# Kernel optimization log

Hardware: AMD Instinct MI355X
Metric: run time of the kernel (lower is better)

The kernel has to match this reference:

```python
import jax, jax.numpy as jnp
import numpy as np

HID = 128
N_NODES = 50000
N_EDGES = 640000
N_GRAPHS = 64
N_LAYERS = 3
LN_EPS = 1e-5


def _ln(h, g, b):
    mu = jnp.mean(h, axis=-1, keepdims=True)
    v = jnp.mean(jnp.square(h - mu), axis=-1, keepdims=True)
    return (h - mu) * jax.lax.rsqrt(v + LN_EPS) * g + b


def _mlp2(h, W1, b1, g, be, W2, b2):
    # Linear -> ReLU -> LayerNorm -> (Dropout=identity in eval) -> Linear
    h = _ln(jax.nn.relu(h @ W1.T + b1), g, be)
    return h @ W2.T + b2


def _forward(x, edge_index, batch, axis_W1, axis_b1, axis_g, axis_be, axis_W2, axis_b2, org_W1, org_b1, org_g, org_be, org_W2, org_b2, nin_W, nin_b, conv_W1, conv_b1, conv_g, conv_be, conv_W2, conv_b2, eps, ln_g, ln_b, gate_W1, gate_b1, gate_g, gate_be, gate_W2, gate_b2, head_W1, head_b1, head_g, head_be, head_W2, head_b2):
    axis = x[:, 9:12]
    origin = x[:, 12:15]
    others = jnp.concatenate([x[:, :9], x[:, 15:19]], axis=1)  # [N, 13]
    axis_z = _mlp2(axis, axis_W1, axis_b1, axis_g, axis_be, axis_W2, axis_b2)
    org_z = _mlp2(origin, org_W1, org_b1, org_g, org_be, org_W2, org_b2)
    h = jnp.concatenate([others, axis_z, org_z], axis=1) @ nin_W.T + nin_b  # [N, HID]
    src, dst = edge_index[0], edge_index[1]
    n = x.shape[0]
    for l in range(N_LAYERS):
        res = h
        # GIN: sum-aggregate source features into targets (gather + scatter-add)
        agg = jax.ops.segment_sum(h[src], dst, num_segments=n)
        m = (1.0 + eps[l]) * h + agg
        m = _mlp2(m, conv_W1[l], conv_b1[l], conv_g[l], conv_be[l], conv_W2[l], conv_b2[l])
        h = _ln(jax.nn.relu(m), ln_g[l], ln_b[l]) + res
    # AttentionalAggregation: segment softmax over per-graph node gates
    gate = _mlp2(h, gate_W1, gate_b1, gate_g, gate_be, gate_W2, gate_b2)  # [N, 1]
    gmax = jax.ops.segment_max(gate, batch, num_segments=N_GRAPHS)
    e = jnp.exp(gate - gmax[batch])
    denom = jax.ops.segment_sum(e, batch, num_segments=N_GRAPHS)
    attn = e / denom[batch]
    g = jax.ops.segment_sum(attn * h, batch, num_segments=N_GRAPHS)  # [B, HID]
    logit = _mlp2(g, head_W1, head_b1, head_g, head_be, head_W2, head_b2)[:, 0]
    return logit


def setup_inputs() -> dict:
    key = jax.random.key(0)
    ks = iter(jax.random.split(key, 64))
    nk = lambda: next(ks)
    lin = lambda o, i: jax.random.normal(nk(), (o, i), jnp.float32) / np.float32(np.sqrt(i))
    lin3 = lambda L, o, i: jnp.stack([lin(o, i) for _ in range(L)])
    z = lambda *s: jnp.zeros(s, jnp.float32)
    o = lambda *s: jnp.ones(s, jnp.float32)
    inp = {}
    inp['x'] = jax.random.normal(nk(), (N_NODES, 19), jnp.float32)
    inp['edge_index'] = jax.random.randint(nk(), (2, N_EDGES), 0, N_NODES)
    inp['batch'] = jnp.sort(jax.random.randint(nk(), (N_NODES,), 0, N_GRAPHS))
    for p in ('axis', 'org'):
        inp[p + '_W1'] = lin(16, 3); inp[p + '_b1'] = z(16)
        inp[p + '_g'] = o(16); inp[p + '_be'] = z(16)
        inp[p + '_W2'] = lin(16, 16); inp[p + '_b2'] = z(16)
    inp['nin_W'] = lin(HID, 45); inp['nin_b'] = z(HID)
    inp['conv_W1'] = lin3(N_LAYERS, HID, HID); inp['conv_b1'] = z(N_LAYERS, HID)
    inp['conv_g'] = o(N_LAYERS, HID); inp['conv_be'] = z(N_LAYERS, HID)
    inp['conv_W2'] = lin3(N_LAYERS, HID, HID); inp['conv_b2'] = z(N_LAYERS, HID)
    inp['eps'] = z(N_LAYERS)
    inp['ln_g'] = o(N_LAYERS, HID); inp['ln_b'] = z(N_LAYERS, HID)
    for p in ('gate', 'head'):
        inp[p + '_W1'] = lin(HID // 2, HID); inp[p + '_b1'] = z(HID // 2)
        inp[p + '_g'] = o(HID // 2); inp[p + '_be'] = z(HID // 2)
        inp[p + '_W2'] = lin(1, HID // 2); inp[p + '_b2'] = z(1)
    return inp


def reference(x, edge_index, batch, axis_W1, axis_b1, axis_g, axis_be, axis_W2, axis_b2, org_W1, org_b1, org_g, org_be, org_W2, org_b2, nin_W, nin_b, conv_W1, conv_b1, conv_g, conv_be, conv_W2, conv_b2, eps, ln_g, ln_b, gate_W1, gate_b1, gate_g, gate_be, gate_W2, gate_b2, head_W1, head_b1, head_g, head_be, head_W2, head_b2):
    return _forward(x, edge_index, batch, axis_W1, axis_b1, axis_g, axis_be, axis_W2, axis_b2, org_W1, org_b1, org_g, org_be, org_W2, org_b2, nin_W, nin_b, conv_W1, conv_b1, conv_g, conv_be, conv_W2, conv_b2, eps, ln_g, ln_b, gate_W1, gate_b1, gate_g, gate_be, gate_W2, gate_b2, head_W1, head_b1, head_g, head_be, head_W2, head_b2)
```

## Files before the change

### kernel.cpp

```cpp
#include <hip/hip_runtime.h>

#define N_NODESC 50000
#define N_EDGESC 640000
#define N_GRAPHSC 64
#define HIDC 128
#define LN_EPSF 1e-5f
#define POOL_SPLIT 16
#define SCAN_NB 49
#define EGRID ((N_EDGESC + 255) / 256)
#define NGRID_GB ((N_NODESC + 255) / 256)
#define PREP_ELEMS (8192 + 49152 + 49152)
#define WPREP_NB ((PREP_ELEMS + 255) / 256)

typedef short bf16x8 __attribute__((ext_vector_type(8)));
typedef float f32x4 __attribute__((ext_vector_type(4)));

static __device__ __forceinline__ unsigned ord_enc(float f) {
  unsigned u = __float_as_uint(f);
  return (u & 0x80000000u) ? ~u : (u | 0x80000000u);
}
static __device__ __forceinline__ float ord_dec(unsigned u) {
  return __uint_as_float((u & 0x80000000u) ? (u ^ 0x80000000u) : ~u);
}
static __device__ __forceinline__ unsigned short f2bf(float x) {
  unsigned u = __float_as_uint(x);
  u += 0x7fffu + ((u >> 16) & 1u);
  return (unsigned short)(u >> 16);
}
static __device__ __forceinline__ float bf2f(unsigned short b) {
  return __uint_as_float(((unsigned)b) << 16);
}

static __device__ __forceinline__ void mlp16(float in0, float in1, float in2,
    const float* __restrict__ W1, const float* __restrict__ b1,
    const float* __restrict__ g, const float* __restrict__ be,
    const float* __restrict__ W2, const float* __restrict__ b2,
    float* __restrict__ out) {
  float h[16];
  float s1 = 0.f, s2 = 0.f;
#pragma unroll
  for (int j = 0; j < 16; ++j) {
    float v = b1[j] + W1[j*3+0]*in0 + W1[j*3+1]*in1 + W1[j*3+2]*in2;
    v = fmaxf(v, 0.f);
    h[j] = v; s1 += v; s2 += v*v;
  }
  float mu = s1 * (1.f/16.f);
  float var = fmaxf(s2 * (1.f/16.f) - mu*mu, 0.f);
  float rs = rsqrtf(var + LN_EPSF);
  float z[16];
#pragma unroll
  for (int j = 0; j < 16; ++j) z[j] = (h[j]-mu)*rs*g[j] + be[j];
#pragma unroll
  for (int j = 0; j < 16; ++j) {
    float v = b2[j];
#pragma unroll
    for (int k = 0; k < 16; ++k) v += W2[j*16+k]*z[k];
    out[j] = v;
  }
}

__global__ __launch_bounds__(256) void hist_gbound_kernel(const int* __restrict__ ei,
    int* __restrict__ deg, const int* __restrict__ batch, int* __restrict__ gstart,
    const float* __restrict__ ninW, unsigned short* __restrict__ ninWb,
    const float* __restrict__ cW1, unsigned short* __restrict__ cW1b,
    const float* __restrict__ cW2, unsigned short* __restrict__ cW2b) {
  const int b = blockIdx.x;
  if (b < EGRID) {
    int e = b * 256 + threadIdx.x;
    if (e < N_EDGESC) atomicAdd(&deg[ei[N_EDGESC + e]], 1);
  } else if (b < EGRID + NGRID_GB) {
    int i = (b - EGRID) * 256 + threadIdx.x;
    if (i >= N_NODESC) return;
    int bb = batch[i];
    int prev = (i == 0) ? -1 : batch[i-1];
    for (int g = prev + 1; g <= bb; ++g) gstart[g] = i;
    if (i == N_NODESC - 1) {
      for (int g = bb + 1; g <= N_GRAPHSC; ++g) gstart[g] = N_NODESC;
    }
  } else {
    int i = (b - EGRID - NGRID_GB) * 256 + threadIdx.x;
    if (i < 8192) {
      int f = i >> 6, k = i & 63;
      ninWb[i] = (k < 45) ? f2bf(ninW[f*45 + k]) : (unsigned short)0;
    } else if (i < 8192 + 49152) {
      int j = i - 8192;
      cW1b[j] = f2bf(cW1[j]);
    } else if (i < PREP_ELEMS) {
      int j = i - 8192 - 49152;
      cW2b[j] = f2bf(cW2[j]);
    }
  }
}

__global__ __launch_bounds__(1024) void scan1_kernel(const int* __restrict__ deg,
                                                     int* __restrict__ incl,
                                                     int* __restrict__ bsum) {
  const int b = blockIdx.x, t = threadIdx.x;
  const int i = b * 1024 + t;
  const int lane = t & 63, w = t >> 6;
  int v = (i < N_NODESC) ? deg[i] : 0;
#pragma unroll
  for (int off = 1; off < 64; off <<= 1) {
    int n = __shfl_up(v, off);
    if (lane >= off) v += n;
  }
  __shared__ int wsum[16];
  if (lane == 63) wsum[w] = v;
  __syncthreads();
  if (t == 0) {
    int run = 0;
#pragma unroll
    for (int k = 0; k < 16; ++k) { int x = wsum[k]; wsum[k] = run; run += x; }
  }
  __syncthreads();
  v += wsum[w];
  if (i < N_NODESC) incl[i] = v;
  if (t == 1023) bsum[b] = v;
}

__global__ __launch_bounds__(1024) void scan23_kernel(const int* __restrict__ deg,
                                                      const int* __restrict__ bsum,
                                                      int* __restrict__ rowptr,
                                                      int* __restrict__ cursor) {
  __shared__ int ex[SCAN_NB + 1];
  const int b = blockIdx.x, t = threadIdx.x;
  if (t < 64) {
    int v = (t < SCAN_NB) ? bsum[t] : 0;
    const int orig = v;
#pragma unroll
    for (int off = 1; off < 64; off <<= 1) {
      int n = __shfl_up(v, off);
      if (t >= off) v += n;
    }
    if (t < SCAN_NB) ex[t] = v - orig;
    if (t == SCAN_NB - 1) ex[SCAN_NB] = v;
  }
  __syncthreads();
  const int i = b * 1024 + t;
  if (i < N_NODESC) {
    int excl = rowptr[i] - deg[i] + ex[b];
    rowptr[i] = excl;
    cursor[i] = excl;
  }
  if (b == 0 && t == 0) rowptr[N_NODESC] = ex[SCAN_NB];
}

__global__ __launch_bounds__(256) void scatter_kernel(const int* __restrict__ ei,
                                                      int* __restrict__ cursor,
                                                      int* __restrict__ esrc) {
  int e = blockIdx.x * 256 + threadIdx.x;
  if (e < N_EDGESC) {
    int d = ei[N_EDGESC + e];
    int slot = atomicAdd(&cursor[d], 1);
    esrc[slot] = ei[e];
  }
}

__global__ __launch_bounds__(256, 4) void enc_mfma_kernel(
    const float* __restrict__ x,
    const float* __restrict__ aW1, const float* __restrict__ ab1,
    const float* __restrict__ ag,  const float* __restrict__ abe,
    const float* __restrict__ aW2, const float* __restrict__ ab2,
    const float* __restrict__ oW1, const float* __restrict__ ob1,
    const float* __restrict__ og,  const float* __restrict__ obe,
    const float* __restrict__ oW2, const float* __restrict__ ob2,
    const unsigned short* __restrict__ ninWb, const float* __restrict__ ninb,
    unsigned short* __restrict__ Hb) {
  __shared__ unsigned short Ab[64*136];
  const int t = threadIdx.x;
  const int nb = blockIdx.x * 64;

  if (t < 192) {
    const int n = t & 63;
    const int gn = nb + n;
    const int grp = t >> 6;
    if (gn < N_NODESC) {
      const float* xr = x + gn * 19;
      if (grp == 0) {
        float z[16];
        mlp16(xr[9], xr[10], xr[11], aW1, ab1, ag, abe, aW2, ab2, z);
#pragma unroll
        for (int k = 0; k < 16; ++k) Ab[n*136 + 13 + k] = f2bf(z[k]);
      } else if (grp == 1) {
        float z[16];
        mlp16(xr[12], xr[13], xr[14], oW1, ob1, og, obe, oW2, ob2, z);
#pragma unroll
        for (int k = 0; k < 16; ++k) Ab[n*136 + 29 + k] = f2bf(z[k]);
      } else {
#pragma unroll
        for (int k = 0; k < 9; ++k) Ab[n*136 + k] = f2bf(xr[k]);
#pragma unroll
        for (int k = 0; k < 4; ++k) Ab[n*136 + 9 + k] = f2bf(xr[15 + k]);
#pragma unroll
        for (int k = 45; k < 64; ++k) Ab[n*136 + k] = 0;
      }
    } else {
      if (grp == 0) {
#pragma unroll
        for (int k = 0; k < 16; ++k) Ab[n*136 + 13 + k] = 0;
      } else if (grp == 1) {
#pragma unroll
        for (int k = 0; k < 16; ++k) Ab[n*136 + 29 + k] = 0;
      } else {
#pragma unroll
        for (int k = 0; k < 13; ++k) Ab[n*136 + k] = 0;
#pragma unroll
        for (int k = 45; k < 64; ++k) Ab[n*136 + k] = 0;
      }
    }
  }
  __syncthreads();

  const int lane = t & 63, wv = t >> 6;
  const int quad = lane >> 4, l16 = lane & 15;
  const int arow = (wv*16 + l16)*136 + quad*8;
  f32x4 acc[8];
#pragma unroll
  for (int ft = 0; ft < 8; ++ft) acc[ft] = (f32x4){0.f,0.f,0.f,0.f};
#pragma unroll
  for (int ks = 0; ks < 2; ++ks) {
    bf16x8 a = *(const bf16x8*)(const void*)&Ab[arow + ks*32];
#pragma unroll
    for (int ft = 0; ft < 8; ++ft) {
      bf16x8 bfr = *(const bf16x8*)&ninWb[(ft*16 + l16)*64 + quad*8 + ks*32];
      acc[ft] = __builtin_amdgcn_mfma_f32_16x16x32_bf16(a, bfr, acc[ft], 0, 0, 0);
    }
  }
  float bb[8];
#pragma unroll
  for (int ft = 0; ft < 8; ++ft) bb[ft] = ninb[ft*16 + l16];
  __syncthreads();
#pragma unroll
  for (int r = 0; r < 4; ++r) {
    int nloc = wv*16 + quad*4 + r;
#pragma unroll
    for (int ft = 0; ft < 8; ++ft)
      Ab[nloc*136 + ft*16 + l16] = f2bf(acc[ft][r] + bb[ft]);
  }
  __syncthreads();
#pragma unroll
  for (int i = 0; i < 4; ++i) {
    int chunk = t + i*256;
    int n = chunk >> 4, c8 = chunk & 15;
    int gn = nb + n;
    if (gn < N_NODESC)
      *(bf16x8*)&Hb[gn*HIDC + c8*8] = *(const bf16x8*)&Ab[n*136 + c8*8];
  }
}

__global__ __launch_bounds__(128) void agg_kernel(const unsigned short* __restrict__ Hb,
    const int* __restrict__ rowptr, const int* __restrict__ esrc,
    const float* __restrict__ epsp, unsigned short* __restrict__ Mb) {
  const int t = threadIdx.x;
  const int c8 = t & 15;
  const int v  = t >> 4;
  const int node = blockIdx.x * 8 + v;
  if (node >= N_NODESC) return;
  const float e1 = 1.0f + epsp[0];
  bf16x8 h = *(const bf16x8*)&Hb[node*HIDC + c8*8];
  float acc[8];
#pragma unroll
  for (int k = 0; k < 8; ++k) acc[k] = 0.f;
  int s = rowptr[node];
  const int e = rowptr[node+1];
  for (; s + 4 <= e; s += 4) {
    int i0 = esrc[s], i1 = esrc[s+1], i2 = esrc[s+2], i3 = esrc[s+3];
    bf16x8 x0 = *(const bf16x8*)&Hb[i0*HIDC + c8*8];
    bf16x8 x1 = *(const bf16x8*)&Hb[i1*HIDC + c8*8];
    bf16x8 x2 = *(const bf16x8*)&Hb[i2*HIDC + c8*8];
    bf16x8 x3 = *(const bf16x8*)&Hb[i3*HIDC + c8*8];
#pragma unroll
    for (int k = 0; k < 8; ++k)
      acc[k] += (bf2f((unsigned short)x0[k]) + bf2f((unsigned short)x1[k]))
              + (bf2f((unsigned short)x2[k]) + bf2f((unsigned short)x3[k]));
  }
  for (; s < e; ++s) {
    bf16x8 x0 = *(const bf16x8*)&Hb[esrc[s]*HIDC + c8*8];
#pragma unroll
    for (int k = 0; k < 8; ++k) acc[k] += bf2f((unsigned short)x0[k]);
  }
  bf16x8 m8;
#pragma unroll
  for (int k = 0; k < 8; ++k)
    m8[k] = (short)f2bf(e1*bf2f((unsigned short)h[k]) + acc[k]);
  *(bf16x8*)&Mb[node*HIDC + c8*8] = m8;
}

__global__ __launch_bounds__(256, 3) void gemmpair_kernel(
    const unsigned short* __restrict__ Mb,
    const unsigned short* __restrict__ Hin,
    const unsigned short* __restrict__ W1b, const float* __restrict__ b1,
    const float* __restrict__ g1, const float* __restrict__ be1,
    const unsigned short* __restrict__ W2b, const float* __restrict__ b2,
    const float* __restrict__ lng, const float* __restrict__ lnb,
    unsigned short* __restrict__ Hout) {
  __shared__ unsigned short Ab[64*136];
  __shared__ unsigned short Wl[128*136];
  const int t = threadIdx.x;
  const int nb = blockIdx.x * 64;

#pragma unroll
  for (int i = 0; i < 4; ++i) {
    int chunk = t + i*256;
    int n = chunk >> 4, c8 = chunk & 15;
    int gn = nb + n;
    bf16x8 v = {0,0,0,0,0,0,0,0};
    if (gn < N_NODESC) v = *(const bf16x8*)&Mb[gn*HIDC + c8*8];
    *(bf16x8*)&Ab[n*136 + c8*8] = v;
  }
#pragma unroll
  for (int i = 0; i < 8; ++i) {
    int q = t + i*256;
    int f = q >> 4, c8 = q & 15;
    *(bf16x8*)&Wl[f*136 + c8*8] = *(const bf16x8*)&W1b[f*HIDC + c8*8];
  }
  __syncthreads();

  const int lane = t & 63, wv = t >> 6;
  const int quad = lane >> 4, l16 = lane & 15;
  const int arow = (wv*16 + l16)*136 + quad*8;

  f32x4 acc[8];
#pragma unroll
  for (int ft = 0; ft < 8; ++ft) acc[ft] = (f32x4){0.f,0.f,0.f,0.f};
#pragma unroll
  for (int ks = 0; ks < 4; ++ks) {
    bf16x8 a = *(const bf16x8*)(const void*)&Ab[arow + ks*32];
#pragma unroll
    for (int ft = 0; ft < 8; ++ft) {
      bf16x8 b = *(const bf16x8*)(const void*)&Wl[(ft*16 + l16)*136 + quad*8 + ks*32];
      acc[ft] = __builtin_amdgcn_mfma_f32_16x16x32_bf16(a, b, acc[ft], 0, 0, 0);
    }
  }

  {
    float bb[8], gg[8], bee[8];
#pragma unroll
    for (int ft = 0; ft < 8; ++ft) {
      int f = ft*16 + l16;
      bb[ft] = b1[f]; gg[ft] = g1[f]; bee[ft] = be1[f];
    }
    float s1[4] = {0,0,0,0}, s2[4] = {0,0,0,0};
#pragma unroll
    for (int ft = 0; ft < 8; ++ft)
#pragma unroll
      for (int r = 0; r < 4; ++r) {
        float v = fmaxf(acc[ft][r] + bb[ft], 0.f);
        acc[ft][r] = v; s1[r] += v; s2[r] += v*v;
      }
#pragma unroll
    for (int m = 1; m < 16; m <<= 1)
#pragma unroll
      for (int r = 0; r < 4; ++r) {
        s1[r] += __shfl_xor(s1[r], m);
        s2[r] += __shfl_xor(s2[r], m);
      }
    float mu[4], rs[4];
#pragma unroll
    for (int r = 0; r < 4; ++r) {
      mu[r] = s1[r] * (1.f/128.f);
      float var = fmaxf(s2[r] * (1.f/128.f) - mu[r]*mu[r], 0.f);
      rs[r] = rsqrtf(var + LN_EPSF);
    }
    __syncthreads();
#pragma unroll
    for (int r = 0; r < 4; ++r) {
      int nloc = wv*16 + quad*4 + r;
#pragma unroll
      for (int ft = 0; ft < 8; ++ft) {
        float o = (acc[ft][r] - mu[r])*rs[r]*gg[ft] + bee[ft];
        Ab[nloc*136 + ft*16 + l16] = f2bf(o);
      }
    }
  }
#pragma unroll
  for (int i = 0; i < 8; ++i) {
    int q = t + i*256;
    int f = q >> 4, c8 = q & 15;
    *(bf16x8*)&Wl[f*136 + c8*8] = *(const bf16x8*)&W2b[f*HIDC + c8*8];
  }
  __syncthreads();

#pragma unroll
  for (int ft = 0; ft < 8; ++ft) acc[ft] = (f32x4){0.f,0.f,0.f,0.f};
#pragma unroll
  for (int ks = 0; ks < 4; ++ks) {
    bf16x8 a = *(const bf16x8*)(const void*)&Ab[arow + ks*32];
#pragma unroll
    for (int ft = 0; ft < 8; ++ft) {
      bf16x8 b = *(const bf16x8*)(const void*)&Wl[(ft*16 + l16)*136 + quad*8 + ks*32];
      acc[ft] = __builtin_amdgcn_mfma_f32_16x16x32_bf16(a, b, acc[ft], 0, 0, 0);
    }
  }

  {
    float bb[8], gg[8], bee[8];
#pragma unroll
    for (int ft = 0; ft < 8; ++ft) {
      int f = ft*16 + l16;
      bb[ft] = b2[f]; gg[ft] = lng[f]; bee[ft] = lnb[f];
    }
    float s1[4] = {0,0,0,0}, s2[4] = {0,0,0,0};
#pragma unroll
    for (int ft = 0; ft < 8; ++ft)
#pragma unroll
      for (int r = 0; r < 4; ++r) {
        float v = fmaxf(acc[ft][r] + bb[ft], 0.f);
        acc[ft][r] = v; s1[r] += v; s2[r] += v*v;
      }
#pragma unroll
    for (int m = 1; m < 16; m <<= 1)
#pragma unroll
      for (int r = 0; r < 4; ++r) {
        s1[r] += __shfl_xor(s1[r], m);
        s2[r] += __shfl_xor(s2[r], m);
      }
    float mu[4], rs[4];
#pragma unroll
    for (int r = 0; r < 4; ++r) {
      mu[r] = s1[r] * (1.f/128.f);
      float var = fmaxf(s2[r] * (1.f/128.f) - mu[r]*mu[r], 0.f);
      rs[r] = rsqrtf(var + LN_EPSF);
    }
    __syncthreads();
#pragma unroll
    for (int r = 0; r < 4; ++r) {
      int nloc = wv*16 + quad*4 + r;
#pragma unroll
      for (int ft = 0; ft < 8; ++ft) {
        float o = (acc[ft][r] - mu[r])*rs[r]*gg[ft] + bee[ft];
        Ab[nloc*136 + ft*16 + l16] = f2bf(o);
      }
    }
  }
  __syncthreads();
#pragma unroll
  for (int i = 0; i < 4; ++i) {
    int chunk = t + i*256;
    int n = chunk >> 4, cc = chunk & 15;
    int gn = nb + n;
    if (gn >= N_NODESC) continue;
    bf16x8 vv = *(const bf16x8*)&Ab[n*136 + cc*8];
    bf16x8 rr = *(const bf16x8*)&Hin[gn*HIDC + cc*8];
    bf16x8 o8;
#pragma unroll
    for (int k = 0; k < 8; ++k)
      o8[k] = (short)f2bf(bf2f((unsigned short)vv[k]) + bf2f((unsigned short)rr[k]));
    *(bf16x8*)&Hout[gn*HIDC + cc*8] = o8;
  }
}

__global__ __launch_bounds__(256, 4) void gate_mfma_kernel(
    const unsigned short* __restrict__ Hb, const float* __restrict__ W1,
    const float* __restrict__ b1, const float* __restrict__ lng,
    const float* __restrict__ lnb, const float* __restrict__ W2,
    const float* __restrict__ b2, const int* __restrict__ batch,
    float* __restrict__ gateb, unsigned* __restrict__ gmaxu) {
  __shared__ unsigned short Ab[64*136];
  __shared__ unsigned short Wl[64*136];
  __shared__ unsigned sgm[N_GRAPHSC];
  const int t = threadIdx.x;
  const int nb = blockIdx.x * 64;
  if (t < N_GRAPHSC) sgm[t] = 0u;
#pragma unroll
  for (int i = 0; i < 4; ++i) {
    int chunk = t + i*256;
    int n = chunk >> 4, c8 = chunk & 15;
    int gn = nb + n;
    bf16x8 v = {0,0,0,0,0,0,0,0};
    if (gn < N_NODESC) v = *(const bf16x8*)&Hb[gn*HIDC + c8*8];
    *(bf16x8*)&Ab[n*136 + c8*8] = v;
  }
#pragma unroll
  for (int i = 0; i < 8; ++i) {
    int q = t + i*256;
    int f = q >> 5, c4 = q & 31;
    float4 v = *(const float4*)&W1[f*HIDC + c4*4];
    ushort4 h;
    h.x = f2bf(v.x); h.y = f2bf(v.y); h.z = f2bf(v.z); h.w = f2bf(v.w);
    *(ushort4*)&Wl[f*136 + c4*4] = h;
  }
  __syncthreads();

  const int lane = t & 63, wv = t >> 6;
  const int quad = lane >> 4, l16 = lane & 15;
  f32x4 acc[4];
#pragma unroll
  for (int ft = 0; ft < 4; ++ft) acc[ft] = (f32x4){0.f,0.f,0.f,0.f};

  const int arow = (wv*16 + l16)*136 + quad*8;
#pragma unroll
  for (int ks = 0; ks < 4; ++ks) {
    bf16x8 a = *(const bf16x8*)(const void*)&Ab[arow + ks*32];
#pragma unroll
    for (int ft = 0; ft < 4; ++ft) {
      bf16x8 b = *(const bf16x8*)(const void*)&Wl[(ft*16 + l16)*136 + quad*8 + ks*32];
      acc[ft] = __builtin_amdgcn_mfma_f32_16x16x32_bf16(a, b, acc[ft], 0, 0, 0);
    }
  }

  float bb[4], gg[4], bee[4], w2v[4];
#pragma unroll
  for (int ft = 0; ft < 4; ++ft) {
    int f = ft*16 + l16;
    bb[ft] = b1[f]; gg[ft] = lng[f]; bee[ft] = lnb[f]; w2v[ft] = W2[f];
  }
  float s1[4] = {0,0,0,0}, s2[4] = {0,0,0,0};
#pragma unroll
  for (int ft = 0; ft < 4; ++ft)
#pragma unroll
    for (int r = 0; r < 4; ++r) {
      float v = fmaxf(acc[ft][r] + bb[ft], 0.f);
      acc[ft][r] = v; s1[r] += v; s2[r] += v*v;
    }
#pragma unroll
  for (int m = 1; m < 16; m <<= 1)
#pragma unroll
    for (int r = 0; r < 4; ++r) {
      s1[r] += __shfl_xor(s1[r], m);
      s2[r] += __shfl_xor(s2[r], m);
    }
  float pd[4];
#pragma unroll
  for (int r = 0; r < 4; ++r) {
    float mu = s1[r] * (1.f/64.f);
    float var = fmaxf(s2[r] * (1.f/64.f) - mu*mu, 0.f);
    float rs = rsqrtf(var + LN_EPSF);
    float p = 0.f;
#pragma unroll
    for (int ft = 0; ft < 4; ++ft)
      p += ((acc[ft][r] - mu)*rs*gg[ft] + bee[ft]) * w2v[ft];
    pd[r] = p;
  }
#pragma unroll
  for (int m = 1; m < 16; m <<= 1)
#pragma unroll
    for (int r = 0; r < 4; ++r) pd[r] += __shfl_xor(pd[r], m);
  if (l16 == 0) {
    float b2v = b2[0];
#pragma unroll
    for (int r = 0; r < 4; ++r) {
      int node = nb + wv*16 + quad*4 + r;
      if (node < N_NODESC) {
        float gv = pd[r] + b2v;
        gateb[node] = gv;
        atomicMax(&sgm[batch[node]], ord_enc(gv));
      }
    }
  }
  __syncthreads();
  if (t < N_GRAPHSC && sgm[t] != 0u) atomicMax(&gmaxu[t], sgm[t]);
}

__global__ __launch_bounds__(256) void pool_kernel(const unsigned short* __restrict__ Hb,
    const float* __restrict__ gateb, const int* __restrict__ gstart,
    const unsigned* __restrict__ gmaxu, float* __restrict__ S,
    float* __restrict__ denom) {
  const int g    = blockIdx.x / POOL_SPLIT;
  const int part = blockIdx.x % POOL_SPLIT;
  const int s0 = gstart[g], s1 = gstart[g+1];
  const int cnt = s1 - s0;
  const int chunk = (cnt + POOL_SPLIT - 1) / POOL_SPLIT;
  int lo = s0 + part * chunk;
  int hi = lo + chunk; if (hi > s1) hi = s1;
  const int t = threadIdx.x;
  const int c8 = t & 15;
  const int v  = t >> 4;
  const float gm = ord_dec(gmaxu[g]);
  float acc[8];
#pragma unroll
  for (int k = 0; k < 8; ++k) acc[k] = 0.f;
  float de = 0.f;
  for (int n = lo + v; n < hi; n += 16) {
    float e = expf(gateb[n] - gm);
    bf16x8 hv = *(const bf16x8*)&Hb[n*HIDC + c8*8];
#pragma unroll
    for (int k = 0; k < 8; ++k) acc[k] += e * bf2f((unsigned short)hv[k]);
    if (c8 == 0) de += e;
  }
  __shared__ float sacc[16*128];
  __shared__ float sden[16];
#pragma unroll
  for (int k = 0; k < 8; ++k) sacc[v*128 + c8*8 + k] = acc[k];
  if (c8 == 0) sden[v] = de;
  __syncthreads();
  if (t < 128) {
    float s = 0.f;
#pragma unroll
    for (int vv = 0; vv < 16; ++vv) s += sacc[vv*128 + t];
    atomicAdd(&S[g*HIDC + t], s);
  }
  if (t == 0) {
    float d = 0.f;
#pragma unroll
    for (int vv = 0; vv < 16; ++vv) d += sden[vv];
    atomicAdd(&denom[g], d);
  }
}

__global__ __launch_bounds__(64) void head_kernel(const float* __restrict__ S,
    const float* __restrict__ denom, const float* __restrict__ W1,
    const float* __restrict__ b1, const float* __restrict__ g,
    const float* __restrict__ be, const float* __restrict__ W2,
    const float* __restrict__ b2, float* __restrict__ out) {
  const int gr = blockIdx.x;
  const int j = threadIdx.x;
  const float inv = 1.0f / denom[gr];
  float v = b1[j];
  for (int k = 0; k < HIDC; ++k) v += (S[gr*HIDC + k] * inv) * W1[j*HIDC + k];
  v = fmaxf(v, 0.f);
  float s1 = v, s2 = v*v;
  for (int off = 32; off; off >>= 1) { s1 += __shfl_xor(s1, off); s2 += __shfl_xor(s2, off); }
  float mu = s1 * (1.f/64.f);
  float var = fmaxf(s2 * (1.f/64.f) - mu*mu, 0.f);
  float rs = rsqrtf(var + LN_EPSF);
  float z = (v-mu)*rs*g[j] + be[j];
  float p = z * W2[j];
  for (int off = 32; off; off >>= 1) p += __shfl_xor(p, off);
  if (j == 0) out[gr] = p + b2[0];
}

extern "C" void kernel_launch(void* const* d_in, const int* in_sizes, int n_in,
                              void* d_out, int out_size, void* d_ws, size_t ws_size,
                              hipStream_t stream) {
  (void)in_sizes; (void)n_in; (void)out_size; (void)ws_size;
  const float* x     = (const float*)d_in[0];
  const int*   ei    = (const int*)d_in[1];
  const int*   batch = (const int*)d_in[2];
  const float* aW1 = (const float*)d_in[3];
  const float* ab1 = (const float*)d_in[4];
  const float* ag  = (const float*)d_in[5];
  const float* abe = (const float*)d_in[6];
  const float* aW2 = (const float*)d_in[7];
  const float* ab2 = (const float*)d_in[8];
  const float* oW1 = (const float*)d_in[9];
  const float* ob1 = (const float*)d_in[10];
  const float* og  = (const float*)d_in[11];
  const float* obe = (const float*)d_in[12];
  const float* oW2 = (const float*)d_in[13];
  const float* ob2 = (const float*)d_in[14];
  const float* ninW = (const float*)d_in[15];
  const float* ninb = (const float*)d_in[16];
  const float* cW1 = (const float*)d_in[17];
  const float* cb1 = (const float*)d_in[18];
  const float* cg  = (const float*)d_in[19];
  const float* cbe = (const float*)d_in[20];
  const float* cW2 = (const float*)d_in[21];
  const float* cb2 = (const float*)d_in[22];
  const float* eps = (const float*)d_in[23];
  const float* lng = (const float*)d_in[24];
  const float* lnb = (const float*)d_in[25];
  const float* gW1 = (const float*)d_in[26];
  const float* gb1 = (const float*)d_in[27];
  const float* gg  = (const float*)d_in[28];
  const float* gbe = (const float*)d_in[29];
  const float* gW2 = (const float*)d_in[30];
  const float* gb2 = (const float*)d_in[31];
  const float* hW1 = (const float*)d_in[32];
  const float* hb1 = (const float*)d_in[33];
  const float* hg  = (const float*)d_in[34];
  const float* hbe = (const float*)d_in[35];
  const float* hW2 = (const float*)d_in[36];
  const float* hb2 = (const float*)d_in[37];

  char* ws = (char*)d_ws;
  unsigned short* Ha = (unsigned short*)(ws + 0);
  unsigned short* Hc = (unsigned short*)(ws + 12800000);
  unsigned short* Mb = (unsigned short*)(ws + 25600000);
  float* gateb = (float*)(ws + 38400000);
  int*   deg   = (int*)(ws + 38600000);
  float* S     = (float*)(ws + 38800000);
  float* denom = (float*)(ws + 38832768);
  unsigned* gmaxu = (unsigned*)(ws + 38833024);
  int* rowptr  = (int*)(ws + 38833280);
  int* cursor  = (int*)(ws + 39033284);
  int* esrc    = (int*)(ws + 39233284);
  int* bsum    = (int*)(ws + 41793284);
  int* gstart  = (int*)(ws + 41793540);
  unsigned short* ninWb = (unsigned short*)(ws + 41800000);
  unsigned short* cW1b  = (unsigned short*)(ws + 41816384);
  unsigned short* cW2b  = (unsigned short*)(ws + 41914688);

  hipMemsetAsync(deg, 0, 233280, stream);

  hist_gbound_kernel<<<EGRID + NGRID_GB + WPREP_NB, 256, 0, stream>>>(
      ei, deg, batch, gstart, ninW, ninWb, cW1, cW1b, cW2, cW2b);
  scan1_kernel<<<SCAN_NB, 1024, 0, stream>>>(deg, rowptr, bsum);
  scan23_kernel<<<SCAN_NB, 1024, 0, stream>>>(deg, bsum, rowptr, cursor);
  scatter_kernel<<<EGRID, 256, 0, stream>>>(ei, cursor, esrc);

  const int ngrid64 = (N_NODESC + 63) / 64;
  enc_mfma_kernel<<<ngrid64, 256, 0, stream>>>(x, aW1, ab1, ag, abe, aW2, ab2,
                                               oW1, ob1, og, obe, oW2, ob2,
                                               ninWb, ninb, Ha);
  unsigned short* cur = Ha;
  unsigned short* nxt = Hc;
  for (int l = 0; l < 3; ++l) {
    agg_kernel<<<(N_NODESC + 7) / 8, 128, 0, stream>>>(cur, rowptr, esrc, eps + l, Mb);
    gemmpair_kernel<<<ngrid64, 256, 0, stream>>>(
        Mb, cur,
        cW1b + l*HIDC*HIDC, cb1 + l*HIDC, cg + l*HIDC, cbe + l*HIDC,
        cW2b + l*HIDC*HIDC, cb2 + l*HIDC, lng + l*HIDC, lnb + l*HIDC,
        nxt);
    unsigned short* tmp = cur; cur = nxt; nxt = tmp;
  }
  gate_mfma_kernel<<<ngrid64, 256, 0, stream>>>(cur, gW1, gb1, gg, gbe, gW2, gb2,
                                                batch, gateb, gmaxu);
  pool_kernel<<<N_GRAPHSC * POOL_SPLIT, 256, 0, stream>>>(cur, gateb, gstart, gmaxu, S, denom);
  head_kernel<<<N_GRAPHSC, 64, 0, stream>>>(S, denom, hW1, hb1, hg, hbe, hW2, hb2,
                                            (float*)d_out);
}
```

Measured before the change: 365.4 us.

## Fuse GIN aggregation into layer GEMM kernel, merge gate MLP and scatter/encoder

```diff
diff --git a/kernel.cpp b/kernel.cpp
--- a/kernel.cpp
+++ b/kernel.cpp
@@ -9,6 +9,7 @@
 #define SCAN_NB 49
 #define EGRID ((N_EDGESC + 255) / 256)
 #define NGRID_GB ((N_NODESC + 255) / 256)
+#define NGRID64 ((N_NODESC + 63) / 64)
 #define PREP_ELEMS (8192 + 49152 + 49152)
 #define WPREP_NB ((PREP_ELEMS + 255) / 256)
 
@@ -145,18 +146,8 @@
   if (b == 0 && t == 0) rowptr[N_NODESC] = ex[SCAN_NB];
 }
 
-__global__ __launch_bounds__(256) void scatter_kernel(const int* __restrict__ ei,
-                                                      int* __restrict__ cursor,
-                                                      int* __restrict__ esrc) {
-  int e = blockIdx.x * 256 + threadIdx.x;
-  if (e < N_EDGESC) {
-    int d = ei[N_EDGESC + e];
-    int slot = atomicAdd(&cursor[d], 1);
-    esrc[slot] = ei[e];
-  }
-}
-
-__global__ __launch_bounds__(256, 4) void enc_mfma_kernel(
+__global__ __launch_bounds__(256, 4) void scatter_enc_kernel(
+    const int* __restrict__ ei, int* __restrict__ cursor, int* __restrict__ esrc,
     const float* __restrict__ x,
     const float* __restrict__ aW1, const float* __restrict__ ab1,
     const float* __restrict__ ag,  const float* __restrict__ abe,
@@ -168,6 +159,17 @@
     unsigned short* __restrict__ Hb) {
   __shared__ unsigned short Ab[64*136];
   const int t = threadIdx.x;
+
+  if (blockIdx.x >= NGRID64) {
+    int e = (blockIdx.x - NGRID64) * 256 + t;
+    if (e < N_EDGESC) {
+      int d = ei[N_EDGESC + e];
+      int slot = atomicAdd(&cursor[d], 1);
+      esrc[slot] = ei[e];
+    }
+    return;
+  }
+
   const int nb = blockIdx.x * 64;
 
   if (t < 192) {
@@ -248,71 +250,73 @@
   }
 }
 
-__global__ __launch_bounds__(128) void agg_kernel(const unsigned short* __restrict__ Hb,
+template<bool GATE>
+__global__ __launch_bounds__(256, 3) void layer_kernel(
+    const unsigned short* __restrict__ Hin,
     const int* __restrict__ rowptr, const int* __restrict__ esrc,
-    const float* __restrict__ epsp, unsigned short* __restrict__ Mb) {
-  const int t = threadIdx.x;
-  const int c8 = t & 15;
-  const int v  = t >> 4;
-  const int node = blockIdx.x * 8 + v;
-  if (node >= N_NODESC) return;
-  const float e1 = 1.0f + epsp[0];
-  bf16x8 h = *(const bf16x8*)&Hb[node*HIDC + c8*8];
-  float acc[8];
-#pragma unroll
-  for (int k = 0; k < 8; ++k) acc[k] = 0.f;
-  int s = rowptr[node];
-  const int e = rowptr[node+1];
-  for (; s + 4 <= e; s += 4) {
-    int i0 = esrc[s], i1 = esrc[s+1], i2 = esrc[s+2], i3 = esrc[s+3];
-    bf16x8 x0 = *(const bf16x8*)&Hb[i0*HIDC + c8*8];
-    bf16x8 x1 = *(const bf16x8*)&Hb[i1*HIDC + c8*8];
-    bf16x8 x2 = *(const bf16x8*)&Hb[i2*HIDC + c8*8];
-    bf16x8 x3 = *(const bf16x8*)&Hb[i3*HIDC + c8*8];
-#pragma unroll
-    for (int k = 0; k < 8; ++k)
-      acc[k] += (bf2f((unsigned short)x0[k]) + bf2f((unsigned short)x1[k]))
-              + (bf2f((unsigned short)x2[k]) + bf2f((unsigned short)x3[k]));
-  }
-  for (; s < e; ++s) {
-    bf16x8 x0 = *(const bf16x8*)&Hb[esrc[s]*HIDC + c8*8];
-#pragma unroll
-    for (int k = 0; k < 8; ++k) acc[k] += bf2f((unsigned short)x0[k]);
-  }
-  bf16x8 m8;
-#pragma unroll
-  for (int k = 0; k < 8; ++k)
-    m8[k] = (short)f2bf(e1*bf2f((unsigned short)h[k]) + acc[k]);
-  *(bf16x8*)&Mb[node*HIDC + c8*8] = m8;
-}
-
-__global__ __launch_bounds__(256, 3) void gemmpair_kernel(
-    const unsigned short* __restrict__ Mb,
-    const unsigned short* __restrict__ Hin,
+    const float* __restrict__ epsp,
     const unsigned short* __restrict__ W1b, const float* __restrict__ b1,
     const float* __restrict__ g1, const float* __restrict__ be1,
     const unsigned short* __restrict__ W2b, const float* __restrict__ b2,
     const float* __restrict__ lng, const float* __restrict__ lnb,
-    unsigned short* __restrict__ Hout) {
+    unsigned short* __restrict__ Hout,
+    const float* __restrict__ gW1, const float* __restrict__ gb1,
+    const float* __restrict__ glng, const float* __restrict__ glnb,
+    const float* __restrict__ gW2, const float* __restrict__ gb2,
+    const int* __restrict__ batch, float* __restrict__ gateb,
+    unsigned* __restrict__ gmaxu) {
   __shared__ unsigned short Ab[64*136];
   __shared__ unsigned short Wl[128*136];
+  __shared__ unsigned sgm[N_GRAPHSC];
   const int t = threadIdx.x;
   const int nb = blockIdx.x * 64;
-
-#pragma unroll
-  for (int i = 0; i < 4; ++i) {
-    int chunk = t + i*256;
-    int n = chunk >> 4, c8 = chunk & 15;
-    int gn = nb + n;
-    bf16x8 v = {0,0,0,0,0,0,0,0};
-    if (gn < N_NODESC) v = *(const bf16x8*)&Mb[gn*HIDC + c8*8];
-    *(bf16x8*)&Ab[n*136 + c8*8] = v;
-  }
+  if (GATE && t < N_GRAPHSC) sgm[t] = 0u;
+
 #pragma unroll
   for (int i = 0; i < 8; ++i) {
     int q = t + i*256;
-    int f = q >> 4, c8 = q & 15;
-    *(bf16x8*)&Wl[f*136 + c8*8] = *(const bf16x8*)&W1b[f*HIDC + c8*8];
+    int f = q >> 4, cc = q & 15;
+    *(bf16x8*)&Wl[f*136 + cc*8] = *(const bf16x8*)&W1b[f*HIDC + cc*8];
+  }
+
+  {
+    const float e1 = 1.0f + epsp[0];
+    const int c8 = t & 15;
+    const int nv = t >> 4;
+#pragma unroll
+    for (int p = 0; p < 4; ++p) {
+      const int n = p*16 + nv;
+      const int gn = nb + n;
+      bf16x8 m8 = {0,0,0,0,0,0,0,0};
+      if (gn < N_NODESC) {
+        bf16x8 h = *(const bf16x8*)&Hin[gn*HIDC + c8*8];
+        float acc[8];
+#pragma unroll
+        for (int k = 0; k < 8; ++k) acc[k] = 0.f;
+        int s = rowptr[gn];
+        const int e = rowptr[gn+1];
+        for (; s + 4 <= e; s += 4) {
+          int i0 = esrc[s], i1 = esrc[s+1], i2 = esrc[s+2], i3 = esrc[s+3];
+          bf16x8 x0 = *(const bf16x8*)&Hin[i0*HIDC + c8*8];
+          bf16x8 x1 = *(const bf16x8*)&Hin[i1*HIDC + c8*8];
+          bf16x8 x2 = *(const bf16x8*)&Hin[i2*HIDC + c8*8];
+          bf16x8 x3 = *(const bf16x8*)&Hin[i3*HIDC + c8*8];
+#pragma unroll
+          for (int k = 0; k < 8; ++k)
+            acc[k] += (bf2f((unsigned short)x0[k]) + bf2f((unsigned short)x1[k]))
+                    + (bf2f((unsigned short)x2[k]) + bf2f((unsigned short)x3[k]));
+        }
+        for (; s < e; ++s) {
+          bf16x8 x0 = *(const bf16x8*)&Hin[esrc[s]*HIDC + c8*8];
+#pragma unroll
+          for (int k = 0; k < 8; ++k) acc[k] += bf2f((unsigned short)x0[k]);
+        }
+#pragma unroll
+        for (int k = 0; k < 8; ++k)
+          m8[k] = (short)f2bf(e1*bf2f((unsigned short)h[k]) + acc[k]);
+      }
+      *(bf16x8*)&Ab[n*136 + c8*8] = m8;
+    }
   }
   __syncthreads();
 
@@ -376,8 +380,8 @@
 #pragma unroll
   for (int i = 0; i < 8; ++i) {
     int q = t + i*256;
-    int f = q >> 4, c8 = q & 15;
-    *(bf16x8*)&Wl[f*136 + c8*8] = *(const bf16x8*)&W2b[f*HIDC + c8*8];
+    int f = q >> 4, cc = q & 15;
+    *(bf16x8*)&Wl[f*136 + cc*8] = *(const bf16x8*)&W2b[f*HIDC + cc*8];
   }
   __syncthreads();
 
@@ -439,117 +443,95 @@
     int chunk = t + i*256;
     int n = chunk >> 4, cc = chunk & 15;
     int gn = nb + n;
-    if (gn >= N_NODESC) continue;
-    bf16x8 vv = *(const bf16x8*)&Ab[n*136 + cc*8];
-    bf16x8 rr = *(const bf16x8*)&Hin[gn*HIDC + cc*8];
-    bf16x8 o8;
-#pragma unroll
-    for (int k = 0; k < 8; ++k)
-      o8[k] = (short)f2bf(bf2f((unsigned short)vv[k]) + bf2f((unsigned short)rr[k]));
-    *(bf16x8*)&Hout[gn*HIDC + cc*8] = o8;
-  }
-}
-
-__global__ __launch_bounds__(256, 4) void gate_mfma_kernel(
-    const unsigned short* __restrict__ Hb, const float* __restrict__ W1,
-    const float* __restrict__ b1, const float* __restrict__ lng,
-    const float* __restrict__ lnb, const float* __restrict__ W2,
-    const float* __restrict__ b2, const int* __restrict__ batch,
-    float* __restrict__ gateb, unsigned* __restrict__ gmaxu) {
-  __shared__ unsigned short Ab[64*136];
-  __shared__ unsigned short Wl[64*136];
-  __shared__ unsigned sgm[N_GRAPHSC];
-  const int t = threadIdx.x;
-  const int nb = blockIdx.x * 64;
-  if (t < N_GRAPHSC) sgm[t] = 0u;
-#pragma unroll
-  for (int i = 0; i < 4; ++i) {
-    int chunk = t + i*256;
-    int n = chunk >> 4, c8 = chunk & 15;
-    int gn = nb + n;
-    bf16x8 v = {0,0,0,0,0,0,0,0};
-    if (gn < N_NODESC) v = *(const bf16x8*)&Hb[gn*HIDC + c8*8];
-    *(bf16x8*)&Ab[n*136 + c8*8] = v;
-  }
-#pragma unroll
-  for (int i = 0; i < 8; ++i) {
-    int q = t + i*256;
-    int f = q >> 5, c4 = q & 31;
-    float4 v = *(const float4*)&W1[f*HIDC + c4*4];
-    ushort4 h;
-    h.x = f2bf(v.x); h.y = f2bf(v.y); h.z = f2bf(v.z); h.w = f2bf(v.w);
-    *(ushort4*)&Wl[f*136 + c4*4] = h;
-  }
-  __syncthreads();
-
-  const int lane = t & 63, wv = t >> 6;
-  const int quad = lane >> 4, l16 = lane & 15;
-  f32x4 acc[4];
-#pragma unroll
-  for (int ft = 0; ft < 4; ++ft) acc[ft] = (f32x4){0.f,0.f,0.f,0.f};
-
-  const int arow = (wv*16 + l16)*136 + quad*8;
-#pragma unroll
-  for (int ks = 0; ks < 4; ++ks) {
-    bf16x8 a = *(const bf16x8*)(const void*)&Ab[arow + ks*32];
+    bf16x8 o8 = {0,0,0,0,0,0,0,0};
+    if (gn < N_NODESC) {
+      bf16x8 vv = *(const bf16x8*)&Ab[n*136 + cc*8];
+      bf16x8 rr = *(const bf16x8*)&Hin[gn*HIDC + cc*8];
+#pragma unroll
+      for (int k = 0; k < 8; ++k)
+        o8[k] = (short)f2bf(bf2f((unsigned short)vv[k]) + bf2f((unsigned short)rr[k]));
+      *(bf16x8*)&Hout[gn*HIDC + cc*8] = o8;
+    }
+    if (GATE) *(bf16x8*)&Ab[n*136 + cc*8] = o8;
+  }
+
+  if (GATE) {
+#pragma unroll
+    for (int i = 0; i < 8; ++i) {
+      int q = t + i*256;
+      int f = q >> 5, c4 = q & 31;
+      float4 v = *(const float4*)&gW1[f*HIDC + c4*4];
+      ushort4 hh;
+      hh.x = f2bf(v.x); hh.y = f2bf(v.y); hh.z = f2bf(v.z); hh.w = f2bf(v.w);
+      *(ushort4*)&Wl[f*136 + c4*4] = hh;
+    }
+    __syncthreads();
+
+    f32x4 gacc[4];
+#pragma unroll
+    for (int ft = 0; ft < 4; ++ft) gacc[ft] = (f32x4){0.f,0.f,0.f,0.f};
+#pragma unroll
+    for (int ks = 0; ks < 4; ++ks) {
+      bf16x8 a = *(const bf16x8*)(const void*)&Ab[arow + ks*32];
+#pragma unroll
+      for (int ft = 0; ft < 4; ++ft) {
+        bf16x8 b = *(const bf16x8*)(const void*)&Wl[(ft*16 + l16)*136 + quad*8 + ks*32];
+        gacc[ft] = __builtin_amdgcn_mfma_f32_16x16x32_bf16(a, b, gacc[ft], 0, 0, 0);
+      }
+    }
+
+    float bb[4], gg[4], bee[4], w2v[4];
 #pragma unroll
     for (int ft = 0; ft < 4; ++ft) {
-      bf16x8 b = *(const bf16x8*)(const void*)&Wl[(ft*16 + l16)*136 + quad*8 + ks*32];
-      acc[ft] = __builtin_amdgcn_mfma_f32_16x16x32_bf16(a, b, acc[ft], 0, 0, 0);
-    }
-  }
-
-  float bb[4], gg[4], bee[4], w2v[4];
-#pragma unroll
-  for (int ft = 0; ft < 4; ++ft) {
-    int f = ft*16 + l16;
-    bb[ft] = b1[f]; gg[ft] = lng[f]; bee[ft] = lnb[f]; w2v[ft] = W2[f];
-  }
-  float s1[4] = {0,0,0,0}, s2[4] = {0,0,0,0};
-#pragma unroll
-  for (int ft = 0; ft < 4; ++ft)
+      int f = ft*16 + l16;
+      bb[ft] = gb1[f]; gg[ft] = glng[f]; bee[ft] = glnb[f]; w2v[ft] = gW2[f];
+    }
+    float s1[4] = {0,0,0,0}, s2[4] = {0,0,0,0};
+#pragma unroll
+    for (int ft = 0; ft < 4; ++ft)
+#pragma unroll
+      for (int r = 0; r < 4; ++r) {
+        float v = fmaxf(gacc[ft][r] + bb[ft], 0.f);
+        gacc[ft][r] = v; s1[r] += v; s2[r] += v*v;
+      }
+#pragma unroll
+    for (int m = 1; m < 16; m <<= 1)
+#pragma unroll
+      for (int r = 0; r < 4; ++r) {
+        s1[r] += __shfl_xor(s1[r], m);
+        s2[r] += __shfl_xor(s2[r], m);
+      }
+    float pd[4];
 #pragma unroll
     for (int r = 0; r < 4; ++r) {
-      float v = fmaxf(acc[ft][r] + bb[ft], 0.f);
-      acc[ft][r] = v; s1[r] += v; s2[r] += v*v;
-    }
-#pragma unroll
-  for (int m = 1; m < 16; m <<= 1)
-#pragma unroll
-    for (int r = 0; r < 4; ++r) {
-      s1[r] += __shfl_xor(s1[r], m);
-      s2[r] += __shfl_xor(s2[r], m);
-    }
-  float pd[4];
-#pragma unroll
-  for (int r = 0; r < 4; ++r) {
-    float mu = s1[r] * (1.f/64.f);
-    float var = fmaxf(s2[r] * (1.f/64.f) - mu*mu, 0.f);
-    float rs = rsqrtf(var + LN_EPSF);
-    float p = 0.f;
-#pragma unroll
-    for (int ft = 0; ft < 4; ++ft)
-      p += ((acc[ft][r] - mu)*rs*gg[ft] + bee[ft]) * w2v[ft];
-    pd[r] = p;
-  }
-#pragma unroll
-  for (int m = 1; m < 16; m <<= 1)
-#pragma unroll
-    for (int r = 0; r < 4; ++r) pd[r] += __shfl_xor(pd[r], m);
-  if (l16 == 0) {
-    float b2v = b2[0];
-#pragma unroll
-    for (int r = 0; r < 4; ++r) {
-      int node = nb + wv*16 + quad*4 + r;
-      if (node < N_NODESC) {
-        float gv = pd[r] + b2v;
-        gateb[node] = gv;
-        atomicMax(&sgm[batch[node]], ord_enc(gv));
-      }
-    }
-  }
-  __syncthreads();
-  if (t < N_GRAPHSC && sgm[t] != 0u) atomicMax(&gmaxu[t], sgm[t]);
+      float mu = s1[r] * (1.f/64.f);
+      float var = fmaxf(s2[r] * (1.f/64.f) - mu*mu, 0.f);
+      float rs = rsqrtf(var + LN_EPSF);
+      float p = 0.f;
+#pragma unroll
+      for (int ft = 0; ft < 4; ++ft)
+        p += ((gacc[ft][r] - mu)*rs*gg[ft] + bee[ft]) * w2v[ft];
+      pd[r] = p;
+    }
+#pragma unroll
+    for (int m = 1; m < 16; m <<= 1)
+#pragma unroll
+      for (int r = 0; r < 4; ++r) pd[r] += __shfl_xor(pd[r], m);
+    if (l16 == 0) {
+      float b2v = gb2[0];
+#pragma unroll
+      for (int r = 0; r < 4; ++r) {
+        int node = nb + wv*16 + quad*4 + r;
+        if (node < N_NODESC) {
+          float gv = pd[r] + b2v;
+          gateb[node] = gv;
+          atomicMax(&sgm[batch[node]], ord_enc(gv));
+        }
+      }
+    }
+    __syncthreads();
+    if (t < N_GRAPHSC && sgm[t] != 0u) atomicMax(&gmaxu[t], sgm[t]);
+  }
 }
 
 __global__ __launch_bounds__(256) void pool_kernel(const unsigned short* __restrict__ Hb,
@@ -666,7 +648,6 @@
   char* ws = (char*)d_ws;
   unsigned short* Ha = (unsigned short*)(ws + 0);
   unsigned short* Hc = (unsigned short*)(ws + 12800000);
-  unsigned short* Mb = (unsigned short*)(ws + 25600000);
   float* gateb = (float*)(ws + 38400000);
   int*   deg   = (int*)(ws + 38600000);
   float* S     = (float*)(ws + 38800000);
@@ -687,26 +668,32 @@
       ei, deg, batch, gstart, ninW, ninWb, cW1, cW1b, cW2, cW2b);
   scan1_kernel<<<SCAN_NB, 1024, 0, stream>>>(deg, rowptr, bsum);
   scan23_kernel<<<SCAN_NB, 1024, 0, stream>>>(deg, bsum, rowptr, cursor);
-  scatter_kernel<<<EGRID, 256, 0, stream>>>(ei, cursor, esrc);
-
-  const int ngrid64 = (N_NODESC + 63) / 64;
-  enc_mfma_kernel<<<ngrid64, 256, 0, stream>>>(x, aW1, ab1, ag, abe, aW2, ab2,
-                                               oW1, ob1, og, obe, oW2, ob2,
-                                               ninWb, ninb, Ha);
-  unsigned short* cur = Ha;
-  unsigned short* nxt = Hc;
-  for (int l = 0; l < 3; ++l) {
-    agg_kernel<<<(N_NODESC + 7) / 8, 128, 0, stream>>>(cur, rowptr, esrc, eps + l, Mb);
-    gemmpair_kernel<<<ngrid64, 256, 0, stream>>>(
-        Mb, cur,
-        cW1b + l*HIDC*HIDC, cb1 + l*HIDC, cg + l*HIDC, cbe + l*HIDC,
-        cW2b + l*HIDC*HIDC, cb2 + l*HIDC, lng + l*HIDC, lnb + l*HIDC,
-        nxt);
-    unsigned short* tmp = cur; cur = nxt; nxt = tmp;
-  }
-  gate_mfma_kernel<<<ngrid64, 256, 0, stream>>>(cur, gW1, gb1, gg, gbe, gW2, gb2,
-                                                batch, gateb, gmaxu);
-  pool_kernel<<<N_GRAPHSC * POOL_SPLIT, 256, 0, stream>>>(cur, gateb, gstart, gmaxu, S, denom);
+  scatter_enc_kernel<<<NGRID64 + EGRID, 256, 0, stream>>>(
+      ei, cursor, esrc,
+      x, aW1, ab1, ag, abe, aW2, ab2,
+      oW1, ob1, og, obe, oW2, ob2,
+      ninWb, ninb, Ha);
+
+  layer_kernel<false><<<NGRID64, 256, 0, stream>>>(
+      Ha, rowptr, esrc, eps + 0,
+      cW1b + 0*HIDC*HIDC, cb1 + 0*HIDC, cg + 0*HIDC, cbe + 0*HIDC,
+      cW2b + 0*HIDC*HIDC, cb2 + 0*HIDC, lng + 0*HIDC, lnb + 0*HIDC,
+      Hc,
+      gW1, gb1, gg, gbe, gW2, gb2, batch, gateb, gmaxu);
+  layer_kernel<false><<<NGRID64, 256, 0, stream>>>(
+      Hc, rowptr, esrc, eps + 1,
+      cW1b + 1*HIDC*HIDC, cb1 + 1*HIDC, cg + 1*HIDC, cbe + 1*HIDC,
+      cW2b + 1*HIDC*HIDC, cb2 + 1*HIDC, lng + 1*HIDC, lnb + 1*HIDC,
+      Ha,
+      gW1, gb1, gg, gbe, gW2, gb2, batch, gateb, gmaxu);
+  layer_kernel<true><<<NGRID64, 256, 0, stream>>>(
+      Ha, rowptr, esrc, eps + 2,
+      cW1b + 2*HIDC*HIDC, cb1 + 2*HIDC, cg + 2*HIDC, cbe + 2*HIDC,
+      cW2b + 2*HIDC*HIDC, cb2 + 2*HIDC, lng + 2*HIDC, lnb + 2*HIDC,
+      Hc,
+      gW1, gb1, gg, gbe, gW2, gb2, batch, gateb, gmaxu);
+
+  pool_kernel<<<N_GRAPHSC * POOL_SPLIT, 256, 0, stream>>>(Hc, gateb, gstart, gmaxu, S, denom);
   head_kernel<<<N_GRAPHSC, 64, 0, stream>>>(S, denom, hW1, hb1, hg, hbe, hW2, hb2,
                                             (float*)d_out);
 }
```

Measured after the change: 405.6 us. 11.0% more time.
